# Kernel optimization log

Hardware: AMD Instinct MI355X
Metric: run time of the kernel (lower is better)

The kernel has to match this reference:

```python
import jax, jax.numpy as jnp
import numpy as np
from jax import lax

C = 64
K = 3
RED = 8


def _lrelu(x):
    return jax.nn.leaky_relu(x, 0.1)


def setup_inputs() -> dict:
    key = jax.random.key(0)
    ks = jax.random.split(key, 8)
    b, h, w = 32, 128, 128
    x0 = jax.random.normal(ks[0], (b, C, h, w), dtype=jnp.float32)
    v = jax.random.normal(ks[1], (b, C), dtype=jnp.float32)
    s = 0.05
    # CA layer: two 1x1 convs (no bias) acting on the [b,64] embedding
    ca_w1 = jax.random.normal(ks[2], (C // RED, C), dtype=jnp.float32) * s
    ca_w2 = jax.random.normal(ks[3], (C, C // RED), dtype=jnp.float32) * s
    # kernel-generating MLP: Linear(64,64) -> LeakyReLU -> Linear(64, 64*K*K), no bias
    k_w1 = jax.random.normal(ks[4], (C, C), dtype=jnp.float32) * s
    k_w2 = jax.random.normal(ks[5], (C * K * K, C), dtype=jnp.float32) * s
    # final 1x1 conv (default_conv, bias=True)
    conv_w = jax.random.normal(ks[6], (C, C), dtype=jnp.float32) * s
    conv_b = jax.random.normal(ks[7], (C,), dtype=jnp.float32) * s
    return {"x0": x0, "v": v, "ca_w1": ca_w1, "ca_w2": ca_w2,
            "k_w1": k_w1, "k_w2": k_w2, "conv_w": conv_w, "conv_b": conv_b}


def reference(x0, v, ca_w1, ca_w2, k_w1, k_w2, conv_w, conv_b):
    b, c, h, w = x0.shape
    # Channel attention: sigmoid(W2 @ lrelu(W1 @ v)) gates x0 per (b,c)
    att = jax.nn.sigmoid(_lrelu(v @ ca_w1.T) @ ca_w2.T)  # [b, c]
    out = x0 * att[:, :, None, None]
    # Per-sample, per-channel K x K kernels generated from the embedding
    kern = (_lrelu(v @ k_w1.T) @ k_w2.T).reshape(b * c, 1, K, K)
    p = (K - 1) // 2
    y = lax.conv_general_dilated(
        out.reshape(1, b * c, h, w), kern,
        window_strides=(1, 1), padding=[(p, p), (p, p)],
        feature_group_count=b * c,
        dimension_numbers=("NCHW", "OIHW", "NCHW"))
    y = _lrelu(y).reshape(b, c, h, w)
    # final 1x1 conv with bias
    return jnp.einsum("bchw,oc->bohw", y, conv_w) + conv_b[None, :, None, None]
```

## Files before the change

### kernel.cpp

```cpp
#include <hip/hip_runtime.h>

#define HW 128
#define XBb 16
#define XBf 4
#define KTb 49168
#define LDS_BYTES 52240

typedef __attribute__((ext_vector_type(8))) short  bfrag;
typedef __attribute__((ext_vector_type(16))) float f16x;
typedef __attribute__((ext_vector_type(4)))  float f4;

__device__ __forceinline__ float lrelu(float x) { return x > 0.f ? x : 0.1f * x; }

__device__ __forceinline__ short f2bf(float f) {
    unsigned u = __builtin_bit_cast(unsigned, f);
    u = u + 0x7FFFu + ((u >> 16) & 1u);
    return (short)(u >> 16);
}
__device__ __forceinline__ float bf2f(short s) {
    return __builtin_bit_cast(float, (unsigned)(unsigned short)s << 16);
}

__device__ float g_ktab[32 * 768];
__device__ short g_whi[4096], g_wlo[4096];

__global__ __launch_bounds__(64) void dgfem_prep(
    const float* __restrict__ v, const float* __restrict__ ca_w1,
    const float* __restrict__ ca_w2, const float* __restrict__ k_w1,
    const float* __restrict__ k_w2, const float* __restrict__ conv_w)
{
    const int b = blockIdx.x;
    const int t = threadIdx.x;

    if (b == 32) {
        for (int i = t; i < 4096; i += 64) {
            float wv = conv_w[i];
            short hi = f2bf(wv);
            short lo = f2bf(wv - bf2f(hi));
            g_whi[i] = hi;
            g_wlo[i] = lo;
        }
        return;
    }

    __shared__ float vb[64], t1[8], att[64], t2[64];
    vb[t] = v[b * 64 + t];
    __syncthreads();

    if (t < 8) {
        float s = 0.f;
        for (int j = 0; j < 64; ++j) s += vb[j] * ca_w1[t * 64 + j];
        t1[t] = lrelu(s);
    }
    {
        float s = 0.f;
        for (int j = 0; j < 64; ++j) s += vb[j] * k_w1[t * 64 + j];
        t2[t] = lrelu(s);
    }
    __syncthreads();
    {
        float s = 0.f;
        for (int i = 0; i < 8; ++i) s += t1[i] * ca_w2[t * 8 + i];
        att[t] = 1.f / (1.f + expf(-s));
    }
    __syncthreads();
    for (int r = t; r < 576; r += 64) {
        int c = r / 9, tp = r - c * 9;
        float s = 0.f;
        for (int j = 0; j < 64; ++j) s += t2[j] * k_w2[r * 64 + j];
        int rr = c >> 4, gg = (c >> 3) & 1, jj = c & 7;
        g_ktab[b * 768 + ((rr * 2 + gg) * 8 + jj) * 12 + tp] = s * att[c];
    }
}

__global__ __launch_bounds__(256) void dgfem_main(
    const float* __restrict__ x0, const float* __restrict__ conv_b,
    float* __restrict__ out)
{
    const int t  = threadIdx.x;
    const int w  = t >> 6;
    const int l  = t & 63;
    const int g  = l >> 5;
    const int ln = l & 31;
    const int px = w * 32 + ln;

    const int bid  = blockIdx.x;
    const int orig = (bid & 7) * 512 + (bid >> 3);
    const int b    = orig >> 7;
    const int gy   = orig & 127;

    const int r0 = min(max(gy - 1, 0), 125);
    const int sA = (min(max(gy - 1, 0), 127) - r0) * 128;
    const int sB = (gy - r0) * 128;
    const int sC = (min(gy + 1, 127) - r0) * 128;
    const float rm0 = (gy > 0)   ? 1.f : 0.f;
    const float rm2 = (gy < 127) ? 1.f : 0.f;

    __shared__ __align__(16) char lds[LDS_BYTES];
    float* ldsf = (float*)lds;

    {
        const float* ksrc = g_ktab + b * 768;
        for (int i = t; i < 768; i += 256) {
            int tp = i % 12;
            float val = ksrc[i];
            float rm = (tp < 3) ? rm0 : ((tp < 6) ? 1.f : rm2);
            *(float*)(lds + KTb + i * 4) = (tp < 9) ? val * rm : 0.f;
        }
    }

    const int l16 = l * 16;
    int oq[1]; (void)oq;
    #define SRCOFF(q) ((((q) * 1024 + l16) / 1536) * 65536 + (((q) * 1024 + l16) % 1536))
    const int o0 = SRCOFF(0), o1 = SRCOFF(1), o2 = SRCOFF(2);
    const int o3 = SRCOFF(3), o4 = SRCOFF(4), o5 = SRCOFF(5);
    #undef SRCOFF

    const char* xb = (const char*)x0 + ((size_t)b << 22);

    #define STAGE(rr_, sel_)                                                   \
    {                                                                          \
        const char* base = xb + ((size_t)((rr_) * 16 + w * 4) << 16)           \
                           + (size_t)r0 * 512;                                 \
        char* dstb = lds + XBb + (sel_) * 24576 + w * 6144;                    \
        __builtin_amdgcn_global_load_lds(                                      \
            (const __attribute__((address_space(1))) unsigned*)(base + o0),    \
            (__attribute__((address_space(3))) unsigned*)(dstb), 16, 0, 0);    \
        __builtin_amdgcn_global_load_lds(                                      \
            (const __attribute__((address_space(1))) unsigned*)(base + o1),    \
            (__attribute__((address_space(3))) unsigned*)(dstb + 1024), 16, 0, 0); \
        __builtin_amdgcn_global_load_lds(                                      \
            (const __attribute__((address_space(1))) unsigned*)(base + o2),    \
            (__attribute__((address_space(3))) unsigned*)(dstb + 2048), 16, 0, 0); \
        __builtin_amdgcn_global_load_lds(                                      \
            (const __attribute__((address_space(1))) unsigned*)(base + o3),    \
            (__attribute__((address_space(3))) unsigned*)(dstb + 3072), 16, 0, 0); \
        __builtin_amdgcn_global_load_lds(                                      \
            (const __attribute__((address_space(1))) unsigned*)(base + o4),    \
            (__attribute__((address_space(3))) unsigned*)(dstb + 4096), 16, 0, 0); \
        __builtin_amdgcn_global_load_lds(                                      \
            (const __attribute__((address_space(1))) unsigned*)(base + o5),    \
            (__attribute__((address_space(3))) unsigned*)(dstb + 5120), 16, 0, 0); \
    }

    f16x acc0, acc1;
    #pragma unroll
    for (int i = 0; i < 16; ++i) { acc0[i] = 0.f; acc1[i] = 0.f; }

    const int   woffb = ln * 128 + g * 16;
    const float mLf = (px > 0)   ? 1.f : 0.f;
    const float mRf = (px < 127) ? 1.f : 0.f;

    STAGE(0, 0);
    __syncthreads();

    #pragma unroll 1
    for (int rr = 0; rr < 4; ++rr) {
        const int sel = rr & 1;
        if (rr < 3) STAGE(rr + 1, sel ^ 1);

        const float* xbase = ldsf + (XBf + sel * 6144 + g * 3072 + px - 1);
        const float* bA = xbase + sA;
        const float* bB = xbase + sB;
        const float* bC = xbase + sC;
        const char*  kb = lds + KTb + (rr * 2 + g) * 384;

        bfrag yh, yl;
        #pragma unroll
        for (int j = 0; j < 8; ++j) {
            const f4* kf = (const f4*)(kb + j * 48);
            f4 kA = kf[0], kB = kf[1], kC = kf[2];
            float xL0 = bA[j * 384]     * mLf;
            float xC0 = bA[j * 384 + 1];
            float xR0 = bA[j * 384 + 2] * mRf;
            float xL1 = bB[j * 384]     * mLf;
            float xC1 = bB[j * 384 + 1];
            float xR1 = bB[j * 384 + 2] * mRf;
            float xL2 = bC[j * 384]     * mLf;
            float xC2 = bC[j * 384 + 1];
            float xR2 = bC[j * 384 + 2] * mRf;
            float a = fmaf(kA.x, xL0, fmaf(kA.y, xC0, kA.z * xR0))
                    + fmaf(kA.w, xL1, fmaf(kB.x, xC1, kB.y * xR1))
                    + fmaf(kB.z, xL2, fmaf(kB.w, xC2, kC.x * xR2));
            a = lrelu(a);
            unsigned u  = __builtin_bit_cast(unsigned, a);
            float   hif = __builtin_bit_cast(float, u & 0xFFFF0000u);
            float   lof = a - hif;
            yh[j] = (short)(u >> 16);
            yl[j] = (short)(__builtin_bit_cast(unsigned, lof) >> 16);
        }

        const char* whb = (const char*)g_whi + woffb + rr * 32;
        const char* wlb = (const char*)g_wlo + woffb + rr * 32;
        bfrag whi0 = *(const bfrag*)(whb);
        bfrag whi1 = *(const bfrag*)(whb + 4096);
        bfrag wlo0 = *(const bfrag*)(wlb);
        bfrag wlo1 = *(const bfrag*)(wlb + 4096);

        acc0 = __builtin_amdgcn_mfma_f32_32x32x16_bf16(whi0, yh, acc0, 0, 0, 0);
        acc0 = __builtin_amdgcn_mfma_f32_32x32x16_bf16(whi0, yl, acc0, 0, 0, 0);
        acc0 = __builtin_amdgcn_mfma_f32_32x32x16_bf16(wlo0, yh, acc0, 0, 0, 0);
        acc1 = __builtin_amdgcn_mfma_f32_32x32x16_bf16(whi1, yh, acc1, 0, 0, 0);
        acc1 = __builtin_amdgcn_mfma_f32_32x32x16_bf16(whi1, yl, acc1, 0, 0, 0);
        acc1 = __builtin_amdgcn_mfma_f32_32x32x16_bf16(wlo1, yh, acc1, 0, 0, 0);

        __syncthreads();
    }
    #undef STAGE

    float* ob = out + ((size_t)b << 20) + (size_t)gy * HW + px;
    #pragma unroll
    for (int q = 0; q < 4; ++q) {
        const int obase = 8 * q + 4 * g;
        float4 bv0 = *(const float4*)&conv_b[obase];
        float4 bv1 = *(const float4*)&conv_b[32 + obase];
        const float* b0f = (const float*)&bv0;
        const float* b1f = (const float*)&bv1;
        #pragma unroll
        for (int r2 = 0; r2 < 4; ++r2) {
            ob[(size_t)(obase + r2) * 16384]      = acc0[q * 4 + r2] + b0f[r2];
            ob[(size_t)(32 + obase + r2) * 16384] = acc1[q * 4 + r2] + b1f[r2];
        }
    }
}

extern "C" void kernel_launch(void* const* d_in, const int* in_sizes, int n_in,
                              void* d_out, int out_size, void* d_ws, size_t ws_size,
                              hipStream_t stream) {
    const float* x0     = (const float*)d_in[0];
    const float* v      = (const float*)d_in[1];
    const float* ca_w1  = (const float*)d_in[2];
    const float* ca_w2  = (const float*)d_in[3];
    const float* k_w1   = (const float*)d_in[4];
    const float* k_w2   = (const float*)d_in[5];
    const float* conv_w = (const float*)d_in[6];
    const float* conv_b = (const float*)d_in[7];
    float* outp = (float*)d_out;

    dgfem_prep<<<dim3(33), dim3(64), 0, stream>>>(v, ca_w1, ca_w2, k_w1, k_w2, conv_w);
    dgfem_main<<<dim3(4096), dim3(256), 0, stream>>>(x0, conv_b, outp);
}
```

Before: 90.34 us.

## Process two output rows per block sharing a four-row staged halo

```diff
diff --git a/kernel.cpp b/kernel.cpp
--- a/kernel.cpp
+++ b/kernel.cpp
@@ -3,8 +3,8 @@
 #define HW 128
 #define XBb 16
 #define XBf 4
-#define KTb 49168
-#define LDS_BYTES 52240
+#define KTb 65552
+#define LDS_BYTES 71696
 
 typedef __attribute__((ext_vector_type(8))) short  bfrag;
 typedef __attribute__((ext_vector_type(16))) float f16x;
@@ -73,7 +73,7 @@
     }
 }
 
-__global__ __launch_bounds__(256) void dgfem_main(
+__global__ __launch_bounds__(512) void dgfem_main(
     const float* __restrict__ x0, const float* __restrict__ conv_b,
     float* __restrict__ out)
 {
@@ -82,65 +82,55 @@
     const int l  = t & 63;
     const int g  = l >> 5;
     const int ln = l & 31;
-    const int px = w * 32 + ln;
+    const int G  = w >> 2;
+    const int wv = w & 3;
+    const int px = wv * 32 + ln;
 
     const int bid  = blockIdx.x;
-    const int orig = (bid & 7) * 512 + (bid >> 3);
-    const int b    = orig >> 7;
-    const int gy   = orig & 127;
-
-    const int r0 = min(max(gy - 1, 0), 125);
+    const int orig = (bid & 7) * 256 + (bid >> 3);
+    const int b    = orig >> 6;
+    const int p    = orig & 63;
+    const int gy0  = p * 2;
+    const int gy   = gy0 + G;
+    const int r0   = min(max(gy0 - 1, 0), 124);
+
     const int sA = (min(max(gy - 1, 0), 127) - r0) * 128;
     const int sB = (gy - r0) * 128;
     const int sC = (min(gy + 1, 127) - r0) * 128;
-    const float rm0 = (gy > 0)   ? 1.f : 0.f;
-    const float rm2 = (gy < 127) ? 1.f : 0.f;
 
     __shared__ __align__(16) char lds[LDS_BYTES];
     float* ldsf = (float*)lds;
 
     {
         const float* ksrc = g_ktab + b * 768;
-        for (int i = t; i < 768; i += 256) {
+        const float m0 = (gy0 > 0)       ? 1.f : 0.f;
+        const float m1 = (gy0 + 1 < 127) ? 1.f : 0.f;
+        for (int i = t; i < 768; i += 512) {
             int tp = i % 12;
-            float val = ksrc[i];
-            float rm = (tp < 3) ? rm0 : ((tp < 6) ? 1.f : rm2);
-            *(float*)(lds + KTb + i * 4) = (tp < 9) ? val * rm : 0.f;
-        }
-    }
-
-    const int l16 = l * 16;
-    int oq[1]; (void)oq;
-    #define SRCOFF(q) ((((q) * 1024 + l16) / 1536) * 65536 + (((q) * 1024 + l16) % 1536))
-    const int o0 = SRCOFF(0), o1 = SRCOFF(1), o2 = SRCOFF(2);
-    const int o3 = SRCOFF(3), o4 = SRCOFF(4), o5 = SRCOFF(5);
-    #undef SRCOFF
+            float val = (tp < 9) ? ksrc[i] : 0.f;
+            float f0 = (tp < 3) ? m0 : 1.f;
+            float f1 = (tp >= 6 && tp < 9) ? m1 : 1.f;
+            *(float*)(lds + KTb + i * 4)        = val * f0;
+            *(float*)(lds + KTb + 3072 + i * 4) = val * f1;
+        }
+    }
 
     const char* xb = (const char*)x0 + ((size_t)b << 22);
+    const int   l16 = l * 16;
 
     #define STAGE(rr_, sel_)                                                   \
     {                                                                          \
-        const char* base = xb + ((size_t)((rr_) * 16 + w * 4) << 16)           \
-                           + (size_t)r0 * 512;                                 \
-        char* dstb = lds + XBb + (sel_) * 24576 + w * 6144;                    \
-        __builtin_amdgcn_global_load_lds(                                      \
-            (const __attribute__((address_space(1))) unsigned*)(base + o0),    \
-            (__attribute__((address_space(3))) unsigned*)(dstb), 16, 0, 0);    \
-        __builtin_amdgcn_global_load_lds(                                      \
-            (const __attribute__((address_space(1))) unsigned*)(base + o1),    \
-            (__attribute__((address_space(3))) unsigned*)(dstb + 1024), 16, 0, 0); \
-        __builtin_amdgcn_global_load_lds(                                      \
-            (const __attribute__((address_space(1))) unsigned*)(base + o2),    \
-            (__attribute__((address_space(3))) unsigned*)(dstb + 2048), 16, 0, 0); \
-        __builtin_amdgcn_global_load_lds(                                      \
-            (const __attribute__((address_space(1))) unsigned*)(base + o3),    \
-            (__attribute__((address_space(3))) unsigned*)(dstb + 3072), 16, 0, 0); \
-        __builtin_amdgcn_global_load_lds(                                      \
-            (const __attribute__((address_space(1))) unsigned*)(base + o4),    \
-            (__attribute__((address_space(3))) unsigned*)(dstb + 4096), 16, 0, 0); \
-        __builtin_amdgcn_global_load_lds(                                      \
-            (const __attribute__((address_space(1))) unsigned*)(base + o5),    \
-            (__attribute__((address_space(3))) unsigned*)(dstb + 5120), 16, 0, 0); \
+        _Pragma("unroll")                                                      \
+        for (int u = 0; u < 4; ++u) {                                          \
+            const int cc = 2 * w + (u >> 1);                                   \
+            const int q  = u & 1;                                              \
+            const char* src = xb + ((size_t)((rr_) * 16 + cc) << 16)           \
+                              + (size_t)r0 * 512 + q * 1024 + l16;             \
+            char* dst = lds + XBb + (sel_) * 32768 + cc * 2048 + q * 1024;     \
+            __builtin_amdgcn_global_load_lds(                                  \
+                (const __attribute__((address_space(1))) unsigned*)src,        \
+                (__attribute__((address_space(3))) unsigned*)dst, 16, 0, 0);   \
+        }                                                                      \
     }
 
     f16x acc0, acc1;
@@ -159,26 +149,26 @@
         const int sel = rr & 1;
         if (rr < 3) STAGE(rr + 1, sel ^ 1);
 
-        const float* xbase = ldsf + (XBf + sel * 6144 + g * 3072 + px - 1);
+        const float* xbase = ldsf + (XBf + sel * 8192 + g * 8 * 512 + px - 1);
         const float* bA = xbase + sA;
         const float* bB = xbase + sB;
         const float* bC = xbase + sC;
-        const char*  kb = lds + KTb + (rr * 2 + g) * 384;
+        const char*  kb = lds + KTb + G * 3072 + (rr * 2 + g) * 384;
 
         bfrag yh, yl;
         #pragma unroll
         for (int j = 0; j < 8; ++j) {
             const f4* kf = (const f4*)(kb + j * 48);
             f4 kA = kf[0], kB = kf[1], kC = kf[2];
-            float xL0 = bA[j * 384]     * mLf;
-            float xC0 = bA[j * 384 + 1];
-            float xR0 = bA[j * 384 + 2] * mRf;
-            float xL1 = bB[j * 384]     * mLf;
-            float xC1 = bB[j * 384 + 1];
-            float xR1 = bB[j * 384 + 2] * mRf;
-            float xL2 = bC[j * 384]     * mLf;
-            float xC2 = bC[j * 384 + 1];
-            float xR2 = bC[j * 384 + 2] * mRf;
+            float xL0 = bA[j * 512]     * mLf;
+            float xC0 = bA[j * 512 + 1];
+            float xR0 = bA[j * 512 + 2] * mRf;
+            float xL1 = bB[j * 512]     * mLf;
+            float xC1 = bB[j * 512 + 1];
+            float xR1 = bB[j * 512 + 2] * mRf;
+            float xL2 = bC[j * 512]     * mLf;
+            float xC2 = bC[j * 512 + 1];
+            float xR2 = bC[j * 512 + 2] * mRf;
             float a = fmaf(kA.x, xL0, fmaf(kA.y, xC0, kA.z * xR0))
                     + fmaf(kA.w, xL1, fmaf(kB.x, xC1, kB.y * xR1))
                     + fmaf(kB.z, xL2, fmaf(kB.w, xC2, kC.x * xR2));
@@ -238,5 +228,5 @@
     float* outp = (float*)d_out;
 
     dgfem_prep<<<dim3(33), dim3(64), 0, stream>>>(v, ca_w1, ca_w2, k_w1, k_w2, conv_w);
-    dgfem_main<<<dim3(4096), dim3(256), 0, stream>>>(x0, conv_b, outp);
-}
+    dgfem_main<<<dim3(2048), dim3(512), 0, stream>>>(x0, conv_b, outp);
+}
```

New measurement: 84.58 us. 1.07x faster.
